# Optimization experiments

Hardware: AMD Instinct MI355X
Metric: run time of the kernel (lower is better)

The kernel has to match this reference:

```python
import jax, jax.numpy as jnp
import numpy as np

N_NODES = 2048
UNITS = 64
IN_DIM = 64
K_DIFF = 2  # max_diffusion_step


def _rw_norm_t(adj):
    # random-walk normalize D^{-1}(A+I), then transpose (as in forward())
    a = adj + jnp.eye(adj.shape[0], dtype=adj.dtype)
    d = jnp.sum(a, axis=1)
    d_inv = jnp.where(d > 0, 1.0 / jnp.where(d > 0, d, 1.0), 0.0)
    return (d_inv[:, None] * a).T


def _gconv(x_cat, adj_t, W, b):
    # x_cat: (B, N, F). Chebyshev-like diffusion: x0, A x0, 2 A x1 - x0, ...
    x0 = x_cat
    xs = [x0]
    x1 = jnp.einsum('nm,bmf->bnf', adj_t, x0)
    xs.append(x1)
    for _ in range(2, K_DIFF + 1):
        x2 = 2.0 * jnp.einsum('nm,bmf->bnf', adj_t, x1) - x0
        xs.append(x2)
        x0, x1 = x1, x2
    x = jnp.stack(xs, axis=-1)  # (B, N, F, K+1) -> matches torch permute(3,1,2,0)
    B, N, F, K = x.shape
    x = x.reshape(B * N, F * K)
    out = x @ W + b
    return out.reshape(B, N, -1)


def setup_inputs() -> dict:
    key = jax.random.key(0)
    ks = jax.random.split(key, 6)
    B = 64
    inputs = jax.random.normal(ks[0], (B, N_NODES * IN_DIM), dtype=jnp.float32)
    hx = jax.random.normal(ks[1], (B, N_NODES * UNITS), dtype=jnp.float32)
    adj = jax.random.uniform(ks[2], (N_NODES, N_NODES), dtype=jnp.float32)
    in_sz = IN_DIM + UNITS
    nm = K_DIFF + 1
    scale = float(np.sqrt(2.0 / (in_sz * nm + 2 * UNITS)))  # xavier-ish
    W_ru = jax.random.normal(ks[3], (in_sz * nm, 2 * UNITS), dtype=jnp.float32) * scale
    b_ru = jnp.ones((2 * UNITS,), dtype=jnp.float32)  # bias_start=1.0
    W_c = jax.random.normal(ks[4], (in_sz * nm, UNITS), dtype=jnp.float32) * scale
    b_c = jnp.zeros((UNITS,), dtype=jnp.float32)
    return {"inputs": inputs, "hx": hx, "adj": adj,
            "W_ru": W_ru, "b_ru": b_ru, "W_c": W_c, "b_c": b_c}


def reference(inputs, hx, adj, W_ru, b_ru, W_c, b_c):
    B = inputs.shape[0]
    x = inputs.reshape(B, N_NODES, IN_DIM)
    h = hx.reshape(B, N_NODES, UNITS)
    adj_t = _rw_norm_t(adj)
    # r/u gates via graph conv + sigmoid
    ru = jax.nn.sigmoid(_gconv(jnp.concatenate([x, h], axis=-1), adj_t, W_ru, b_ru))
    r, u = ru[..., :UNITS], ru[..., UNITS:]
    # candidate state
    c = jnp.tanh(_gconv(jnp.concatenate([x, r * h], axis=-1), adj_t, W_c, b_c))
    new_state = u * h + (1.0 - u) * c
    return new_state.reshape(B, N_NODES * UNITS)
```

## Files before the change

kernel.cpp:

```cpp
#include <hip/hip_runtime.h>
#include <math.h>

typedef __attribute__((ext_vector_type(8))) short short8;
typedef __attribute__((ext_vector_type(4))) float float4v;
typedef __attribute__((ext_vector_type(16))) float float16v;
typedef __attribute__((ext_vector_type(4))) unsigned short ushort4v;
typedef unsigned short u16;
typedef unsigned int u32;

#define NB 64
#define NN 2048
#define FD 128
#define UD 64
#define KT 384


__device__ __forceinline__ u16 f2bf(float f) {
    unsigned int u = __float_as_uint(f);
    u += 0x7fffu + ((u >> 16) & 1u);
    return (u16)(u >> 16);
}
__device__ __forceinline__ float bf2f(u16 s) {
    return __uint_as_float(((unsigned int)s) << 16);
}
__device__ __forceinline__ float sigmoidf_(float x) {
    return 1.0f / (1.0f + expf(-x));
}
__device__ __forceinline__ void gl2lds16(const u16* g, u16* l) {
    __builtin_amdgcn_global_load_lds((const __attribute__((address_space(1))) unsigned int*)g,
                                     (__attribute__((address_space(3))) unsigned int*)l,
                                     16, 0, 0);
}

__global__ void k_prep(const float* __restrict__ adj, float* __restrict__ d_inv,
                       const float* __restrict__ W_ru, u16* __restrict__ Wru,
                       const float* __restrict__ W_c,  u16* __restrict__ Wc,
                       const float* __restrict__ x, const float* __restrict__ h,
                       u16* __restrict__ X0f, u16* __restrict__ X0m) {
    __shared__ u16 T[128 * 136];
    int bid = blockIdx.x;
    int t = threadIdx.x;
    if (bid < 2048) {
        int m = bid;
        const float4v* row = (const float4v*)(adj + (size_t)m * NN);
        float s = 0.f;
        for (int i = t; i < NN / 4; i += 256) {
            float4v v = row[i];
            s += v.x + v.y + v.z + v.w;
        }
        float* red = (float*)T;
        for (int off = 32; off; off >>= 1) s += __shfl_down(s, off, 64);
        if ((t & 63) == 0) red[t >> 6] = s;
        __syncthreads();
        if (t == 0) {
            float tt = red[0] + red[1] + red[2] + red[3] + 1.0f;
            d_inv[m] = 1.0f / tt;
        }
        return;
    }
    if (bid < 2336) {
        const float* W; u16* Wt; int OD, idx;
        if (bid < 2240) { W = W_ru; Wt = Wru; OD = FD; idx = (bid - 2048) * 256 + t; }
        else            { W = W_c;  Wt = Wc;  OD = UD; idx = (bid - 2240) * 256 + t; }
        if (idx >= KT * OD) return;
        int o  = idx % OD;
        int kp = idx / OD;
        int kd = kp >> 7, f = kp & 127;
        float v;
        if (kd == 0)      v = W[(size_t)(f * 3 + 0) * OD + o] - W[(size_t)(f * 3 + 2) * OD + o];
        else if (kd == 1) v = W[(size_t)(f * 3 + 1) * OD + o];
        else              v = 2.0f * W[(size_t)(f * 3 + 2) * OD + o];
        size_t dst = ((size_t)(o >> 5) * 12 + (kp >> 5)) * 1024 + (((kp >> 3) & 3) * 32 + (o & 31)) * 8 + (kp & 7);
        Wt[dst] = f2bf(v);
        return;
    }
    int rb = bid - 2336;
    int m0 = (rb & 15) * 128;
    int b  = rb >> 4;
    const float* srcs[2] = { x + (size_t)b * (NN * 64), h + (size_t)b * (NN * 64) };
    for (int s = 0; s < 2; ++s) {
        const float* src = srcs[s];
        for (int p = 0; p < 8; ++p) {
            int idx = t + 256 * p;
            int mi = idx >> 4;
            int f4 = idx & 15;
            float4v v = *(const float4v*)(src + (size_t)(m0 + mi) * 64 + f4 * 4);
            float vv[4] = {v.x, v.y, v.z, v.w};
#pragma unroll
            for (int j = 0; j < 4; ++j)
                T[(s * 64 + f4 * 4 + j) * 136 + mi] = f2bf(vv[j]);
        }
    }
    __syncthreads();
#pragma unroll
    for (int p = 0; p < 8; ++p) {
        int S = t + 256 * p;
        int fgl = S >> 9, kgl = (S >> 7) & 3, s = S & 127;
        int c = s >> 5, r = s & 31;
        short8 v = *(const short8*)(T + (fgl * 32 + r) * 136 + kgl * 32 + c * 8);
        *(short8*)(X0f + ((size_t)(b * 4 + fgl) * 64 + (m0 >> 5) + kgl) * 1024 + s * 8) = v;
    }
#pragma unroll
    for (int p = 0; p < 8; ++p) {
        int S = t + 256 * p;
        int fc = S >> 7;
        int mi = S & 127;
        short8 v;
#pragma unroll
        for (int e = 0; e < 8; ++e) v[e] = (short)T[(fc * 8 + e) * 136 + mi];
        size_t dst = ((size_t)(b * 64 + (m0 >> 5) + (mi >> 5)) * 4 + (fc >> 2)) * 1024
                     + ((fc & 3) * 32 + (mi & 31)) * 8;
        *(short8*)(X0m + dst) = v;
    }
}

__global__ void k_adjT(const float* __restrict__ adj, const float* __restrict__ d_inv,
                       u16* __restrict__ adjT) {
    __shared__ u16 T[64 * 72];
    int m0 = blockIdx.x * 64;
    int n0 = blockIdx.y * 64;
    int t = threadIdx.x;
    for (int p = 0; p < 4; ++p) {
        int idx = t + 256 * p;
        int i  = idx >> 4;
        int n4 = idx & 15;
        int m = m0 + i;
        float4v v = *(const float4v*)(adj + (size_t)m * NN + n0 + n4 * 4);
        float di = d_inv[m];
        float vv[4] = {v.x, v.y, v.z, v.w};
#pragma unroll
        for (int j = 0; j < 4; ++j) {
            int n = n0 + n4 * 4 + j;
            float a = vv[j] + ((m == n) ? 1.0f : 0.0f);
            T[(n4 * 4 + j) * 72 + i] = f2bf(a * di);
        }
    }
    __syncthreads();
#pragma unroll
    for (int p = 0; p < 2; ++p) {
        int S = t + 256 * p;
        int rgl = S >> 8, kgl = (S >> 7) & 1, s = S & 127;
        int c = s >> 5, r = s & 31;
        short8 v = *(const short8*)(T + (rgl * 32 + r) * 72 + kgl * 32 + c * 8);
        *(short8*)(adjT + ((size_t)((n0 >> 5) + rgl) * 64 + (m0 >> 5) + kgl) * 1024 + s * 8) = v;
    }
}

template<int FG>
__global__ __launch_bounds__(256, 4)
void k_gemm(const u16* __restrict__ A, const u16* __restrict__ Bc,
            u16* __restrict__ outF, u16* __restrict__ outM, int cBlocks) {
    __shared__ u16 SM[16384];
    u16* A0 = SM;            u16* A1 = SM + 4096;
    u16* B0 = SM + 8192;     u16* B1 = SM + 12288;

    int id = blockIdx.x + cBlocks * blockIdx.y;
    int band = cBlocks >> 3;
    int g = id & 7, s = id >> 3;
    int cb = g * band + (s % band);
    int nb = s / band;
    int c0 = cb * 128;
    int n0 = nb * 128;

    int t = threadIdx.x;
    int wave = t >> 6, lane = t & 63;
    int wy = wave & 1, wx = wave >> 1;
    int ln = lane & 31, hi = lane >> 5;
    int l16 = lane * 8;

    const u16* gaP[2];
    const u16* gbP[2];
#pragma unroll
    for (int i = 0; i < 2; ++i) {
        int T = t + 256 * i;
        gaP[i] = A  + ((size_t)((n0 >> 5) + (T >> 7)) * 64) * 1024 + (size_t)(T & 127) * 8;
        gbP[i] = Bc + ((size_t)((c0 >> 5) + (T >> 7)) * 64) * 1024 + (size_t)(T & 127) * 8;
    }

    float16v acc[2][2];
#pragma unroll
    for (int i = 0; i < 2; ++i)
#pragma unroll
        for (int j = 0; j < 2; ++j)
#pragma unroll
            for (int e = 0; e < 16; ++e) acc[i][j][e] = 0.f;

#pragma unroll
    for (int i = 0; i < 2; ++i) { gl2lds16(gaP[i], A0 + (t + 256 * i) * 8); gl2lds16(gbP[i], B0 + (t + 256 * i) * 8); }

#pragma unroll 2
    for (int it = 0; it < 64; ++it) {
        u16* Ac = (it & 1) ? A1 : A0;
        u16* Bs = (it & 1) ? B1 : B0;
        __syncthreads();
        if (it + 1 < 64) {
            int ko = (it + 1) * 1024;
            u16* An = (it & 1) ? A0 : A1;
            u16* Bn = (it & 1) ? B0 : B1;
#pragma unroll
            for (int i = 0; i < 2; ++i) { gl2lds16(gaP[i] + ko, An + (t + 256 * i) * 8); gl2lds16(gbP[i] + ko, Bn + (t + 256 * i) * 8); }
        }
        short8 fa[2][2], fb[2][2];
#pragma unroll
        for (int ks = 0; ks < 2; ++ks) {
#pragma unroll
            for (int mt = 0; mt < 2; ++mt)
                fa[ks][mt] = *(const short8*)(Bs + ((wx * 2 + mt) * 2 + ks) * 512 + l16);
#pragma unroll
            for (int nt = 0; nt < 2; ++nt)
                fb[ks][nt] = *(const short8*)(Ac + ((wy * 2 + nt) * 2 + ks) * 512 + l16);
        }
#pragma unroll
        for (int ks = 0; ks < 2; ++ks)
#pragma unroll
            for (int mt = 0; mt < 2; ++mt)
#pragma unroll
                for (int nt = 0; nt < 2; ++nt)
                    acc[mt][nt] = __builtin_amdgcn_mfma_f32_32x32x16_bf16(fa[ks][mt], fb[ks][nt], acc[mt][nt], 0, 0, 0);
    }

#pragma unroll
    for (int mt = 0; mt < 2; ++mt) {
#pragma unroll
        for (int nt = 0; nt < 2; ++nt) {
            int mg = (n0 >> 5) + wy * 2 + nt;
            int batch = (FG == 4) ? cb : (2 * cb + wx);
            int fg = (FG == 4) ? (wx * 2 + mt) : mt;
            size_t pbase = ((size_t)(batch * 64 + mg) * FG + fg) * 1024;
#pragma unroll
            for (int eq = 0; eq < 4; ++eq) {
                ushort4v pk;
#pragma unroll
                for (int r = 0; r < 4; ++r) pk[r] = f2bf(acc[mt][nt][eq * 4 + r]);
                *(ushort4v*)(outM + pbase + (eq * 32 + ln) * 8 + 4 * hi) = pk;
            }
        }
    }

    if (outF) {
        __syncthreads();
#pragma unroll
        for (int p = 0; p < 2; ++p) {
            if (p) __syncthreads();
            if (wx == p) {
#pragma unroll
                for (int mt = 0; mt < 2; ++mt)
#pragma unroll
                    for (int nt = 0; nt < 2; ++nt)
#pragma unroll
                        for (int e = 0; e < 16; ++e) {
                            int cl = mt * 32 + 4 * hi + 8 * (e >> 2) + (e & 3);
                            int nl = wy * 64 + nt * 32 + ln;
                            SM[cl * 136 + nl] = f2bf(acc[mt][nt][e]);
                        }
            }
            __syncthreads();
#pragma unroll
            for (int pp = 0; pp < 4; ++pp) {
                int S = t + 256 * pp;
                int rgl = S >> 9, kgl = (S >> 7) & 3, sl = S & 127;
                int c = sl >> 5, r = sl & 31;
                short8 v = *(const short8*)(SM + (rgl * 32 + r) * 136 + kgl * 32 + c * 8);
                size_t gaddr = ((size_t)((c0 >> 5) + p * 2 + rgl) * 64 + (n0 >> 5) + kgl) * 1024 + sl * 8;
                *(short8*)(outF + gaddr) = v;
            }
        }
    }
}

__global__ __launch_bounds__(256, 3)
void k_proj_ru(const u16* __restrict__ X0m, const u16* __restrict__ X1m, const u16* __restrict__ Ym,
               const u16* __restrict__ Wp, const float* __restrict__ bias, const float* __restrict__ hx,
               u16* __restrict__ RH0f, u16* __restrict__ RH0m, u16* __restrict__ Ut) {
    __shared__ u16 SM[16384];
    u16 *Xa = SM, *Xb = SM + 4096, *Wa = SM + 8192, *Wb = SM + 12288;
    int mb = blockIdx.x, b = blockIdx.y;
    int m0 = mb * 128, mg0 = mb * 4;
    int t = threadIdx.x, wave = t >> 6, lane = t & 63;
    int wx = wave & 1, wyy = wave >> 1;
    int ln = lane & 31, hi = lane >> 5;
    const u16* Xs[3] = {X0m, X1m, Ym};
    int p0 = t >> 7, s0 = t & 127;

    float16v acc[2][2];
#pragma unroll
    for (int i = 0; i < 2; ++i)
#pragma unroll
        for (int j = 0; j < 2; ++j)
#pragma unroll
            for (int e = 0; e < 16; ++e) acc[i][j][e] = 0.f;

    gl2lds16(Xs[0] + ((size_t)((b * 64 + mg0 + p0) * 4)) * 1024 + s0 * 8, Xa + t * 8);
    gl2lds16(Xs[0] + ((size_t)((b * 64 + mg0 + p0 + 2) * 4)) * 1024 + s0 * 8, Xa + (t + 256) * 8);
    gl2lds16(Wp + ((size_t)(p0 * 12)) * 1024 + s0 * 8, Wa + t * 8);
    gl2lds16(Wp + ((size_t)((p0 + 2) * 12)) * 1024 + s0 * 8, Wa + (t + 256) * 8);

    for (int kq = 0; kq < 12; ++kq) {
        u16* Xc = (kq & 1) ? Xb : Xa;
        u16* Wc = (kq & 1) ? Wb : Wa;
        __syncthreads();
        if (kq + 1 < 12) {
            int k2 = kq + 1, kd = k2 >> 2, kg = k2 & 3;
            u16* Xn = (kq & 1) ? Xa : Xb;
            u16* Wn = (kq & 1) ? Wa : Wb;
            const u16* xb = Xs[kd];
            gl2lds16(xb + ((size_t)((b * 64 + mg0 + p0) * 4 + kg)) * 1024 + s0 * 8, Xn + t * 8);
            gl2lds16(xb + ((size_t)((b * 64 + mg0 + p0 + 2) * 4 + kg)) * 1024 + s0 * 8, Xn + (t + 256) * 8);
            gl2lds16(Wp + ((size_t)(p0 * 12 + k2)) * 1024 + s0 * 8, Wn + t * 8);
            gl2lds16(Wp + ((size_t)((p0 + 2) * 12 + k2)) * 1024 + s0 * 8, Wn + (t + 256) * 8);
        }
        short8 fa[2][2], fb[2][2];
#pragma unroll
        for (int ks = 0; ks < 2; ++ks) {
#pragma unroll
            for (int mt = 0; mt < 2; ++mt)
                fa[ks][mt] = *(const short8*)(Xc + ((wx * 2 + mt) * 2 + ks) * 512 + lane * 8);
#pragma unroll
            for (int nt = 0; nt < 2; ++nt)
                fb[ks][nt] = *(const short8*)(Wc + ((wyy * 2 + nt) * 2 + ks) * 512 + lane * 8);
        }
#pragma unroll
        for (int ks = 0; ks < 2; ++ks)
#pragma unroll
            for (int mt = 0; mt < 2; ++mt)
#pragma unroll
                for (int nt = 0; nt < 2; ++nt)
                    acc[mt][nt] = __builtin_amdgcn_mfma_f32_32x32x16_bf16(fa[ks][mt], fb[ks][nt], acc[mt][nt], 0, 0, 0);
    }
    __syncthreads();
    if (wyy == 0) {
#pragma unroll
        for (int mt = 0; mt < 2; ++mt)
#pragma unroll
            for (int nt = 0; nt < 2; ++nt) {
                int o = nt * 32 + ln;
                float bo = bias[o];
                u16 vals[16];
#pragma unroll
                for (int e = 0; e < 16; ++e) {
                    int ml = wx * 64 + mt * 32 + 4 * hi + 8 * (e >> 2) + (e & 3);
                    float sg = sigmoidf_(acc[mt][nt][e] + bo);
                    float hh = hx[((size_t)b * NN + m0 + ml) * 64 + o];
                    vals[e] = f2bf(sg * hh);
                    SM[ml * 76 + o] = vals[e];
                }
#pragma unroll
                for (int eq = 0; eq < 4; ++eq) {
                    ushort4v pk;
#pragma unroll
                    for (int r = 0; r < 4; ++r) pk[r] = vals[eq * 4 + r];
                    size_t addr = ((size_t)(b * 2 + nt) * 64 + mg0 + wx * 2 + mt) * 1024 + (eq * 32 + ln) * 8 + 4 * hi;
                    *(ushort4v*)(RH0f + addr) = pk;
                }
            }
    } else {
#pragma unroll
        for (int mt = 0; mt < 2; ++mt)
#pragma unroll
            for (int nt = 0; nt < 2; ++nt) {
                int og = nt * 32 + ln;
                float bo = bias[64 + og];
#pragma unroll
                for (int e = 0; e < 16; ++e) {
                    int ml = wx * 64 + mt * 32 + 4 * hi + 8 * (e >> 2) + (e & 3);
                    Ut[((size_t)b * NN + m0 + ml) * 64 + og] = f2bf(sigmoidf_(acc[mt][nt][e] + bo));
                }
            }
    }
    __syncthreads();
#pragma unroll
    for (int j = 0; j < 4; ++j) {
        int C = t + 256 * j;
        int p = C >> 7, sl = C & 127;
        int mgl = p >> 1, ug = p & 1;
        int cq = sl >> 5, r = sl & 31;
        short8 v = *(const short8*)(SM + (mgl * 32 + r) * 76 + ug * 32 + cq * 8);
        *(short8*)(RH0m + ((size_t)((b * 64 + mg0 + mgl) * 2 + ug)) * 1024 + sl * 8) = v;
    }
}

__global__ __launch_bounds__(256, 4)
void k_proj_c(const u16* __restrict__ X0m, const u16* __restrict__ X1m, const u16* __restrict__ Ym,
              const u16* __restrict__ RH0m, const u16* __restrict__ RH1m, const u16* __restrict__ Zm,
              const u16* __restrict__ Wp, const float* __restrict__ bias,
              const float* __restrict__ hx, const u16* __restrict__ Ut,
              float* __restrict__ out) {
    __shared__ u16 SM[12288];
    u16 *Xa = SM, *Xb = SM + 4096, *Wa = SM + 8192, *Wb = SM + 10240;
    int mb = blockIdx.x, b = blockIdx.y;
    int m0 = mb * 128, mg0 = mb * 4;
    int t = threadIdx.x, wave = t >> 6, lane = t & 63;
    int wx = wave & 1, wyy = wave >> 1;
    int ln = lane & 31, hi = lane >> 5;
    const u16* Xs[3] = {X0m, X1m, Ym};
    const u16* Rs[3] = {RH0m, RH1m, Zm};
    int p0 = t >> 7, s0 = t & 127;

    float16v acc[2];
#pragma unroll
    for (int i = 0; i < 2; ++i)
#pragma unroll
        for (int e = 0; e < 16; ++e) acc[i][e] = 0.f;

    gl2lds16(Xs[0] + ((size_t)((b * 64 + mg0 + p0) * 4)) * 1024 + s0 * 8, Xa + t * 8);
    gl2lds16(Xs[0] + ((size_t)((b * 64 + mg0 + p0 + 2) * 4)) * 1024 + s0 * 8, Xa + (t + 256) * 8);
    gl2lds16(Wp + ((size_t)(p0 * 12)) * 1024 + s0 * 8, Wa + t * 8);

    for (int kq = 0; kq < 12; ++kq) {
        u16* Xc = (kq & 1) ? Xb : Xa;
        u16* Wc = (kq & 1) ? Wb : Wa;
        __syncthreads();
        if (kq + 1 < 12) {
            int k2 = kq + 1, kd = k2 >> 2, fb2 = (k2 & 3) * 32;
            u16* Xn = (kq & 1) ? Xa : Xb;
            u16* Wn = (kq & 1) ? Wa : Wb;
            const u16* mat; size_t pb0, pb1;
            if (fb2 < 64) {
                mat = Xs[kd];
                pb0 = ((size_t)((b * 64 + mg0 + p0) * 4 + (fb2 >> 5))) * 1024;
                pb1 = ((size_t)((b * 64 + mg0 + p0 + 2) * 4 + (fb2 >> 5))) * 1024;
            } else {
                mat = Rs[kd];
                pb0 = ((size_t)((b * 64 + mg0 + p0) * 2 + ((fb2 >> 5) - 2))) * 1024;
                pb1 = ((size_t)((b * 64 + mg0 + p0 + 2) * 2 + ((fb2 >> 5) - 2))) * 1024;
            }
            gl2lds16(mat + pb0 + s0 * 8, Xn + t * 8);
            gl2lds16(mat + pb1 + s0 * 8, Xn + (t + 256) * 8);
            gl2lds16(Wp + ((size_t)(p0 * 12 + k2)) * 1024 + s0 * 8, Wn + t * 8);
        }
        short8 fa[2][2], fbg[2];
#pragma unroll
        for (int ks = 0; ks < 2; ++ks) {
#pragma unroll
            for (int mt = 0; mt < 2; ++mt)
                fa[ks][mt] = *(const short8*)(Xc + ((wx * 2 + mt) * 2 + ks) * 512 + lane * 8);
            fbg[ks] = *(const short8*)(Wc + (wyy * 2 + ks) * 512 + lane * 8);
        }
#pragma unroll
        for (int ks = 0; ks < 2; ++ks)
#pragma unroll
            for (int mt = 0; mt < 2; ++mt)
                acc[mt] = __builtin_amdgcn_mfma_f32_32x32x16_bf16(fa[ks][mt], fbg[ks], acc[mt], 0, 0, 0);
    }
    int o = wyy * 32 + ln;
    float bo = bias[o];
#pragma unroll
    for (int mt = 0; mt < 2; ++mt)
#pragma unroll
        for (int e = 0; e < 16; ++e) {
            int ml = wx * 64 + mt * 32 + 4 * hi + 8 * (e >> 2) + (e & 3);
            size_t idx = ((size_t)b * NN + m0 + ml) * 64 + o;
            float c = tanhf(acc[mt][e] + bo);
            float u = bf2f(Ut[idx]);
            float hh = hx[idx];
            out[idx] = u * hh + (1.0f - u) * c;
        }
}

extern "C" void kernel_launch(void* const* d_in, const int* in_sizes, int n_in,
                              void* d_out, int out_size, void* d_ws, size_t ws_size,
                              hipStream_t stream) {
    const float* x    = (const float*)d_in[0];
    const float* hx   = (const float*)d_in[1];
    const float* adj  = (const float*)d_in[2];
    const float* W_ru = (const float*)d_in[3];
    const float* b_ru = (const float*)d_in[4];
    const float* W_c  = (const float*)d_in[5];
    const float* b_c  = (const float*)d_in[6];
    float* out = (float*)d_out;

    char* ws = (char*)d_ws;
    size_t off = 0;
    auto alloc = [&](size_t bytes) -> void* {
        void* p = ws + off;
        off += (bytes + 255) & ~(size_t)255;
        return p;
    };
    float* d_inv = (float*)alloc((size_t)NN * 4);
    u16* adjT = (u16*)alloc((size_t)NN * NN * 2);
    u16* Wru  = (u16*)alloc((size_t)FD * KT * 2);
    u16* Wc   = (u16*)alloc((size_t)UD * KT * 2);
    u16* X0f = (u16*)alloc((size_t)NB * FD * NN * 2);
    u16* X1f = (u16*)alloc((size_t)NB * FD * NN * 2);
    u16* X0m = (u16*)alloc((size_t)NB * FD * NN * 2);
    u16* X1m = (u16*)alloc((size_t)NB * FD * NN * 2);
    u16* Ym  = (u16*)alloc((size_t)NB * FD * NN * 2);
    u16* RH0m = (u16*)alloc((size_t)NB * UD * NN * 2);
    u16* RH1m = (u16*)alloc((size_t)NB * UD * NN * 2);
    u16* Zm   = (u16*)alloc((size_t)NB * UD * NN * 2);
    u16* Ut   = (u16*)alloc((size_t)NB * UD * NN * 2);
    u16* RH0f = X0f;
    u16* RH1f = X1f;

    k_prep<<<dim3(3360), dim3(256), 0, stream>>>(adj, d_inv, W_ru, Wru, W_c, Wc, x, hx, X0f, X0m);
    k_adjT<<<dim3(32, 32), dim3(256), 0, stream>>>(adj, d_inv, adjT);
    k_gemm<4><<<dim3(64, 16), dim3(256), 0, stream>>>(adjT, X0f, X1f, X1m, 64);
    k_gemm<4><<<dim3(64, 16), dim3(256), 0, stream>>>(adjT, X1f, nullptr, Ym, 64);
    k_proj_ru<<<dim3(16, NB), dim3(256), 0, stream>>>(X0m, X1m, Ym, Wru, b_ru, hx, RH0f, RH0m, Ut);
    k_gemm<2><<<dim3(32, 16), dim3(256), 0, stream>>>(adjT, RH0f, RH1f, RH1m, 32);
    k_gemm<2><<<dim3(32, 16), dim3(256), 0, stream>>>(adjT, RH1f, nullptr, Zm, 32);
    k_proj_c<<<dim3(16, NB), dim3(256), 0, stream>>>(X0m, X1m, Ym, RH0m, RH1m, Zm, Wc, b_c, hx, Ut, out);
}
```

Baseline: 450.9 us.

## Add 256x256-tile triple-buffered MFMA GEMM kernel for first-stage diffusion

Adds a new k_gemm256 kernel with 512 threads, 256x256 output tiles, a three-stage LDS ring fed by direct global-to-LDS loads, split half-K steps and setprio around the 32x32x16 bf16 MFMAs. It replaces the 128-tile k_gemm for the two large diffusion GEMMs on the x/h features. The aim is more reuse per loaded tile and better overlap of loads with MFMA work. In exchange it uses 96 KB of LDS with two blocks per CU and launches only 256 blocks, which may leave some CUs idle.

```diff
diff --git a/kernel.cpp b/kernel.cpp
--- a/kernel.cpp
+++ b/kernel.cpp
@@ -143,6 +143,156 @@
         int c = s >> 5, r = s & 31;
         short8 v = *(const short8*)(T + (rgl * 32 + r) * 72 + kgl * 32 + c * 8);
         *(short8*)(adjT + ((size_t)((n0 >> 5) + rgl) * 64 + (m0 >> 5) + kgl) * 1024 + s * 8) = v;
+    }
+}
+
+template<int HAS_F>
+__global__ __launch_bounds__(512, 2)
+void k_gemm256(const u16* __restrict__ Ap, const u16* __restrict__ Bc,
+               u16* __restrict__ outF, u16* __restrict__ outM) {
+    __shared__ __align__(16) u16 SM[49152];
+    int bid = blockIdx.x;
+    int nb = bid & 7;
+    int cb = bid >> 3;
+    int n0 = nb * 256, c0 = cb * 256;
+    int t = threadIdx.x;
+    int wave = t >> 6, lane = t & 63;
+    int wx = wave >> 2;
+    int wy = wave & 3;
+    int ln = lane & 31, hi = lane >> 5;
+
+    const u16* gA[2];
+    const u16* gB[2];
+    int la[2], lb[2];
+#pragma unroll
+    for (int i = 0; i < 2; ++i) {
+        int idx = i * 512 + t;
+        int p = idx >> 7, s = idx & 127;
+        gA[i] = Bc + ((size_t)((c0 >> 5) + p) * 64) * 1024 + s * 8;
+        gB[i] = Ap + ((size_t)((n0 >> 5) + p) * 64) * 1024 + s * 8;
+        la[i] = idx * 8;
+        lb[i] = 8192 + idx * 8;
+    }
+
+    float16v acc[4][2];
+#pragma unroll
+    for (int mt = 0; mt < 4; ++mt)
+#pragma unroll
+        for (int nt = 0; nt < 2; ++nt)
+#pragma unroll
+            for (int e = 0; e < 16; ++e) acc[mt][nt][e] = 0.f;
+
+#pragma unroll
+    for (int i = 0; i < 2; ++i) { gl2lds16(gA[i], SM + la[i]); gl2lds16(gB[i], SM + lb[i]); }
+#pragma unroll
+    for (int i = 0; i < 2; ++i) { gl2lds16(gA[i] + 1024, SM + 16384 + la[i]); gl2lds16(gB[i] + 1024, SM + 16384 + lb[i]); }
+    asm volatile("s_waitcnt vmcnt(4)" ::: "memory");
+    __builtin_amdgcn_s_barrier();
+    __builtin_amdgcn_sched_barrier(0);
+
+    int rdA = wx * 4096 + lane * 8;
+    int rdB = 8192 + wy * 2048 + lane * 8;
+
+    int cur = 0;
+    for (int kt = 0; kt < 64; ++kt) {
+        u16* buf = SM + cur * 16384;
+        int stg = cur + 2; if (stg >= 3) stg -= 3;
+        u16* sbuf = SM + stg * 16384;
+        size_t ko = (size_t)(kt + 2) * 1024;
+
+        short8 fa[4], fb[2];
+#pragma unroll
+        for (int mt = 0; mt < 4; ++mt) fa[mt] = *(const short8*)(buf + rdA + mt * 1024);
+#pragma unroll
+        for (int nt = 0; nt < 2; ++nt) fb[nt] = *(const short8*)(buf + rdB + nt * 1024);
+        if (kt < 62) {
+#pragma unroll
+            for (int i = 0; i < 2; ++i) gl2lds16(gA[i] + ko, sbuf + la[i]);
+        }
+        __builtin_amdgcn_s_barrier();
+        asm volatile("s_waitcnt lgkmcnt(0)" ::: "memory");
+        __builtin_amdgcn_sched_barrier(0);
+        __builtin_amdgcn_s_setprio(1);
+#pragma unroll
+        for (int mt = 0; mt < 4; ++mt)
+#pragma unroll
+            for (int nt = 0; nt < 2; ++nt)
+                acc[mt][nt] = __builtin_amdgcn_mfma_f32_32x32x16_bf16(fa[mt], fb[nt], acc[mt][nt], 0, 0, 0);
+        __builtin_amdgcn_s_setprio(0);
+        __builtin_amdgcn_s_barrier();
+        __builtin_amdgcn_sched_barrier(0);
+
+#pragma unroll
+        for (int mt = 0; mt < 4; ++mt) fa[mt] = *(const short8*)(buf + rdA + mt * 1024 + 512);
+#pragma unroll
+        for (int nt = 0; nt < 2; ++nt) fb[nt] = *(const short8*)(buf + rdB + nt * 1024 + 512);
+        if (kt < 62) {
+#pragma unroll
+            for (int i = 0; i < 2; ++i) gl2lds16(gB[i] + ko, sbuf + lb[i]);
+        }
+        __builtin_amdgcn_s_barrier();
+        asm volatile("s_waitcnt lgkmcnt(0)" ::: "memory");
+        __builtin_amdgcn_sched_barrier(0);
+        __builtin_amdgcn_s_setprio(1);
+#pragma unroll
+        for (int mt = 0; mt < 4; ++mt)
+#pragma unroll
+            for (int nt = 0; nt < 2; ++nt)
+                acc[mt][nt] = __builtin_amdgcn_mfma_f32_32x32x16_bf16(fa[mt], fb[nt], acc[mt][nt], 0, 0, 0);
+        __builtin_amdgcn_s_setprio(0);
+        if (kt < 62) asm volatile("s_waitcnt vmcnt(4)" ::: "memory");
+        else         asm volatile("s_waitcnt vmcnt(0)" ::: "memory");
+        __builtin_amdgcn_s_barrier();
+        __builtin_amdgcn_sched_barrier(0);
+
+        cur = (cur == 2) ? 0 : cur + 1;
+    }
+
+    int batch0 = cb * 2 + wx;
+#pragma unroll
+    for (int mt = 0; mt < 4; ++mt) {
+#pragma unroll
+        for (int nt = 0; nt < 2; ++nt) {
+            int mg = (n0 >> 5) + wy * 2 + nt;
+            size_t pbase = ((size_t)(batch0 * 64 + mg) * 4 + mt) * 1024;
+#pragma unroll
+            for (int eq = 0; eq < 4; ++eq) {
+                ushort4v pk;
+#pragma unroll
+                for (int r = 0; r < 4; ++r) pk[r] = f2bf(acc[mt][nt][eq * 4 + r]);
+                *(ushort4v*)(outM + pbase + (eq * 32 + ln) * 8 + 4 * hi) = pk;
+            }
+        }
+    }
+
+    if (HAS_F) {
+#pragma unroll
+        for (int p = 0; p < 2; ++p) {
+            __syncthreads();
+            if ((wy >> 1) == p) {
+#pragma unroll
+                for (int mt = 0; mt < 4; ++mt)
+#pragma unroll
+                    for (int nt = 0; nt < 2; ++nt)
+#pragma unroll
+                        for (int e = 0; e < 16; ++e) {
+                            int cl = wx * 128 + mt * 32 + 4 * hi + 8 * (e >> 2) + (e & 3);
+                            int nl = (wy & 1) * 64 + nt * 32 + ln;
+                            SM[cl * 136 + nl] = f2bf(acc[mt][nt][e]);
+                        }
+            }
+            __syncthreads();
+#pragma unroll
+            for (int j = 0; j < 8; ++j) {
+                int S = t + 512 * j;
+                int col = S >> 4, nd8 = S & 15;
+                short8 v = *(const short8*)(SM + col * 136 + nd8 * 8);
+                int gn = n0 + p * 128 + nd8 * 8;
+                size_t dst = ((size_t)((c0 >> 5) + (col >> 5)) * 64 + (gn >> 5)) * 1024
+                             + (size_t)((((gn >> 3) & 3) * 32 + (col & 31))) * 8;
+                *(short8*)(outF + dst) = v;
+            }
+        }
     }
 }
 
@@ -494,8 +644,8 @@
 
     k_prep<<<dim3(3360), dim3(256), 0, stream>>>(adj, d_inv, W_ru, Wru, W_c, Wc, x, hx, X0f, X0m);
     k_adjT<<<dim3(32, 32), dim3(256), 0, stream>>>(adj, d_inv, adjT);
-    k_gemm<4><<<dim3(64, 16), dim3(256), 0, stream>>>(adjT, X0f, X1f, X1m, 64);
-    k_gemm<4><<<dim3(64, 16), dim3(256), 0, stream>>>(adjT, X1f, nullptr, Ym, 64);
+    k_gemm256<1><<<dim3(256), dim3(512), 0, stream>>>(adjT, X0f, X1f, X1m);
+    k_gemm256<0><<<dim3(256), dim3(512), 0, stream>>>(adjT, X1f, nullptr, Ym);
     k_proj_ru<<<dim3(16, NB), dim3(256), 0, stream>>>(X0m, X1m, Ym, Wru, b_ru, hx, RH0f, RH0m, Ut);
     k_gemm<2><<<dim3(32, 16), dim3(256), 0, stream>>>(adjT, RH0f, RH1f, RH1m, 32);
     k_gemm<2><<<dim3(32, 16), dim3(256), 0, stream>>>(adjT, RH1f, nullptr, Zm, 32);
```

New measurement: 441.6 us. 2.1% less time.
